# Kernel tuning notes

Hardware: AMD Instinct MI355X
Metric: run time of the kernel (lower is better)

Reference implementation:

```python
import jax, jax.numpy as jnp
import numpy as np

DIM = 1024
HEADS = 16
HDIM = DIM // HEADS  # 64
HID = 4096           # mlp_ratio * dim
SCALE = HDIM ** -0.5
EPS = 1e-5           # torch LayerNorm default


def _ln(z, g, b):
    m = jnp.mean(z, axis=-1, keepdims=True)
    v = jnp.var(z, axis=-1, keepdims=True)
    return (z - m) * jax.lax.rsqrt(v + EPS) * g + b


def _forward(x, g1, beta1, Wq, bq, Wk, bk, Wv, bv, Wo, bo, g2, beta2, W1, b1m, W2, b2m,
             window_size, spatial_h, spatial_w):
    B, L, C = x.shape
    ws = window_size
    nh, nw = spatial_h // ws, spatial_w // ws  # grid divisible by window -> pad = 0

    # norm1 + window partition: [B,L,C] -> [B*nh*nw, ws*ws, C]
    h = _ln(x, g1, beta1).reshape(B, spatial_h, spatial_w, C)
    h = h.reshape(B, nh, ws, nw, ws, C).transpose(0, 1, 3, 2, 4, 5)
    h = h.reshape(B * nh * nw, ws * ws, C)
    Bw, N, _ = h.shape

    # separate q/k/v linears, manual scaled-dot-product attention
    q = (h @ Wq + bq).reshape(Bw, N, HEADS, HDIM).transpose(0, 2, 1, 3)
    k = (h @ Wk + bk).reshape(Bw, N, HEADS, HDIM).transpose(0, 2, 1, 3)
    v = (h @ Wv + bv).reshape(Bw, N, HEADS, HDIM).transpose(0, 2, 1, 3)
    attn = jax.nn.softmax(jnp.einsum('bhqd,bhkd->bhqk', q, k) * SCALE, axis=-1)
    o = jnp.einsum('bhqk,bhkd->bhqd', attn, v).transpose(0, 2, 1, 3).reshape(Bw, N, C)
    o = o @ Wo + bo

    # window unpartition back to [B,L,C]
    o = o.reshape(B, nh, nw, ws, ws, C).transpose(0, 1, 3, 2, 4, 5).reshape(B, L, C)

    x = x + o  # residual (drop_path prob = 0)
    h2 = _ln(x, g2, beta2)
    x = x + (jax.nn.gelu(h2 @ W1 + b1m, approximate=False) @ W2 + b2m)
    return x


def setup_inputs() -> dict:
    key = jax.random.key(0)
    ks = jax.random.split(key, 8)
    s = 0.02
    return {
        'x': jax.random.normal(ks[0], (8, 4096, DIM), jnp.float32),
        'g1': jnp.ones((DIM,), jnp.float32),
        'beta1': jnp.zeros((DIM,), jnp.float32),
        'Wq': jax.random.normal(ks[1], (DIM, DIM), jnp.float32) * s,
        'bq': jnp.zeros((DIM,), jnp.float32),
        'Wk': jax.random.normal(ks[2], (DIM, DIM), jnp.float32) * s,
        'bk': jnp.zeros((DIM,), jnp.float32),
        'Wv': jax.random.normal(ks[3], (DIM, DIM), jnp.float32) * s,
        'bv': jnp.zeros((DIM,), jnp.float32),
        'Wo': jax.random.normal(ks[4], (DIM, DIM), jnp.float32) * s,
        'bo': jnp.zeros((DIM,), jnp.float32),
        'g2': jnp.ones((DIM,), jnp.float32),
        'beta2': jnp.zeros((DIM,), jnp.float32),
        'W1': jax.random.normal(ks[5], (DIM, HID), jnp.float32) * s,
        'b1m': jnp.zeros((HID,), jnp.float32),
        'W2': jax.random.normal(ks[6], (HID, DIM), jnp.float32) * s,
        'b2m': jnp.zeros((DIM,), jnp.float32),
        'window_size': 16,
        'spatial_h': 64,
        'spatial_w': 64,
    }


def reference(x, g1, beta1, Wq, bq, Wk, bk, Wv, bv, Wo, bo, g2, beta2, W1, b1m, W2, b2m,
              window_size, spatial_h, spatial_w):
    return _forward(x, g1, beta1, Wq, bq, Wk, bk, Wv, bv, Wo, bo, g2, beta2,
                    W1, b1m, W2, b2m, window_size, spatial_h, spatial_w)
```

## Files before the change

kernel.cpp:

```cpp
#include <hip/hip_runtime.h>
#include <math.h>
#include <stdint.h>

typedef __bf16 bf16;
typedef __bf16 bf16x8 __attribute__((ext_vector_type(8)));
typedef __bf16 bf16x4 __attribute__((ext_vector_type(4)));
typedef float  f32x4  __attribute__((ext_vector_type(4)));

#define MFMA(a,b,c) __builtin_amdgcn_mfma_f32_16x16x32_bf16(a,b,c,0,0,0)

__device__ __forceinline__ float gelu_exact(float z){
    return 0.5f * z * (1.0f + erff(z * 0.70710678118654752f));
}

__device__ __forceinline__ void gload16(const void* g, void* l){
    __builtin_amdgcn_global_load_lds(
        (const __attribute__((address_space(1))) uint32_t*)(uintptr_t)g,
        (__attribute__((address_space(3))) uint32_t*)(uintptr_t)l,
        16, 0, 0);
}

__global__ void wprep(const float* __restrict__ W, bf16* __restrict__ WT, int K, int N)
{
    __shared__ float tile[32][33];
    int tx = threadIdx.x, ty = threadIdx.y;
    int n0 = blockIdx.x * 32, k0 = blockIdx.y * 32;
    for (int j = 0; j < 4; j++)
        tile[ty + j*8][tx] = W[(size_t)(k0 + ty + j*8) * N + n0 + tx];
    __syncthreads();
    for (int j = 0; j < 4; j++)
        WT[(size_t)(n0 + ty + j*8) * K + k0 + tx] = (bf16)tile[tx][ty + j*8];
}

__global__ void bcat(const float* __restrict__ a, const float* __restrict__ b,
                     const float* __restrict__ c, float* __restrict__ o)
{
    int t = blockIdx.x * 256 + threadIdx.x;
    o[t] = t < 1024 ? a[t] : (t < 2048 ? b[t - 1024] : c[t - 2048]);
}

template<int PERM>
__global__ __launch_bounds__(256) void ln_kernel(const float* __restrict__ x,
    const float* __restrict__ g, const float* __restrict__ beta,
    bf16* __restrict__ out)
{
    int rw = blockIdx.x;
    int src = rw;
    if (PERM){
        int w = rw >> 8, p = rw & 255;
        int b = w >> 4, inh = (w >> 2) & 3, inw = w & 3, pi = p >> 4, pj = p & 15;
        src = b * 4096 + (inh*16 + pi) * 64 + inw*16 + pj;
    }
    const float* xr = x + (size_t)src * 1024;
    int t = threadIdx.x;
    float4 xv = ((const float4*)xr)[t];
    float s  = xv.x + xv.y + xv.z + xv.w;
    float sq = xv.x*xv.x + xv.y*xv.y + xv.z*xv.z + xv.w*xv.w;
    for (int m = 1; m < 64; m <<= 1){ s += __shfl_xor(s, m); sq += __shfl_xor(sq, m); }
    __shared__ float red[8];
    int wid = t >> 6, lane = t & 63;
    if (lane == 0){ red[wid] = s; red[4 + wid] = sq; }
    __syncthreads();
    float S  = red[0] + red[1] + red[2] + red[3];
    float SQ = red[4] + red[5] + red[6] + red[7];
    float mean = S * (1.f/1024.f);
    float var  = SQ * (1.f/1024.f) - mean*mean;
    float rstd = rsqrtf(var + 1e-5f);
    float4 gv = ((const float4*)g)[t];
    float4 bv = ((const float4*)beta)[t];
    bf16x4 o;
    o[0] = (bf16)((xv.x - mean) * rstd * gv.x + bv.x);
    o[1] = (bf16)((xv.y - mean) * rstd * gv.y + bv.y);
    o[2] = (bf16)((xv.z - mean) * rstd * gv.z + bv.z);
    o[3] = (bf16)((xv.w - mean) * rstd * gv.w + bv.w);
    *(bf16x4*)(out + (size_t)rw * 1024 + t*4) = o;
}

template<int EPI>
__global__ __launch_bounds__(512, 2) void gemm256(
    const bf16* __restrict__ Ag, const bf16* __restrict__ BT,
    const float* __restrict__ bias, const float* __restrict__ res,
    void* __restrict__ outp, int N, int K)
{
    extern __shared__ char lds[];
    const int KT = K >> 6;
    const int gx = N >> 8;
    int nwg = gridDim.x;
    int id  = blockIdx.x;
    int cpx = nwg >> 3;
    int wg  = (id & 7) * cpx + (id >> 3);
    int bx = wg % gx, by = wg / gx;
    int m0 = by << 8, n0 = bx << 8;

    int t = threadIdx.x;
    int lane = t & 63, wid = t >> 6;
    int wm = wid >> 2, wn = wid & 3;
    int qoff = lane & 15, quad = lane >> 4;

    auto stage = [&](int H){
        int kt = H >> 2, h = H & 3;
        int isA = h >> 1, hh = h & 1;
        char* lb = lds + ((kt & 1) << 16) + (isA << 15) + (hh << 14);
        const bf16* g0 = (isA ? Ag + (size_t)(m0 + (hh << 7)) * K
                              : BT + (size_t)(n0 + (hh << 7)) * K) + (kt << 6);
        #pragma unroll
        for (int ld = 0; ld < 2; ld++){
            int ch  = ld*512 + t;
            int row = ch >> 3;
            int cc  = (ch & 7) ^ (row & 7);
            gload16(g0 + (size_t)row * K + cc*8, lb + (ld*512 + wid*64)*16);
        }
    };

    f32x4 acc[8][4] = {};

    int npro = 4*KT < 7 ? 4*KT : 7;
    for (int H = 0; H < npro; H++) stage(H);
    asm volatile("s_waitcnt vmcnt(6)" ::: "memory");
    __builtin_amdgcn_s_barrier();
    __builtin_amdgcn_sched_barrier(0);

    const int HMAX = 4*KT;
    const char* lA0 = lds + 32768 + (wm << 14) + qoff*128;
    const char* lB0 = lds + ((wn >> 1) << 14) + ((wn & 1) << 13) + qoff*128;
    int p0 = (quad ^ (qoff & 7)) << 4;
    int p1 = p0 ^ 64;

    for (int kt = 0; kt < KT; kt++){
        int bufo = (kt & 1) << 16;
        const char* lA = lA0 + bufo;
        const char* lB = lB0 + bufo;
        bf16x8 a0[8], a1[8], b0[4], b1[4];

        #pragma unroll
        for (int nt = 0; nt < 4; nt++){
            b0[nt] = *(const bf16x8*)(lB + nt*2048 + p0);
            b1[nt] = *(const bf16x8*)(lB + nt*2048 + p1);
        }
        #pragma unroll
        for (int mt = 0; mt < 8; mt++)
            a0[mt] = *(const bf16x8*)(lA + mt*2048 + p0);
        if (4*kt + 7 < HMAX) stage(4*kt + 7);
        __builtin_amdgcn_sched_barrier(0);
        __builtin_amdgcn_s_barrier();
        __builtin_amdgcn_sched_barrier(0);
        __builtin_amdgcn_s_setprio(1);
        #pragma unroll
        for (int mt = 0; mt < 8; mt++){
            acc[mt][0] = MFMA(a0[mt], b0[0], acc[mt][0]);
            acc[mt][1] = MFMA(a0[mt], b0[1], acc[mt][1]);
        }
        __builtin_amdgcn_s_setprio(0);
        __builtin_amdgcn_sched_barrier(0);
        asm volatile("s_waitcnt lgkmcnt(0)" ::: "memory");
        __builtin_amdgcn_s_barrier();
        __builtin_amdgcn_sched_barrier(0);

        #pragma unroll
        for (int mt = 0; mt < 8; mt++)
            a1[mt] = *(const bf16x8*)(lA + mt*2048 + p1);
        if (4*kt + 8 < HMAX) stage(4*kt + 8);
        __builtin_amdgcn_sched_barrier(0);
        __builtin_amdgcn_s_barrier();
        __builtin_amdgcn_sched_barrier(0);
        __builtin_amdgcn_s_setprio(1);
        #pragma unroll
        for (int mt = 0; mt < 8; mt++){
            acc[mt][2] = MFMA(a0[mt], b0[2], acc[mt][2]);
            acc[mt][3] = MFMA(a0[mt], b0[3], acc[mt][3]);
        }
        __builtin_amdgcn_s_setprio(0);
        __builtin_amdgcn_sched_barrier(0);
        __builtin_amdgcn_s_barrier();
        __builtin_amdgcn_sched_barrier(0);

        if (4*kt + 9 < HMAX) stage(4*kt + 9);
        __builtin_amdgcn_sched_barrier(0);
        __builtin_amdgcn_s_barrier();
        __builtin_amdgcn_sched_barrier(0);
        __builtin_amdgcn_s_setprio(1);
        #pragma unroll
        for (int mt = 0; mt < 8; mt++){
            acc[mt][0] = MFMA(a1[mt], b1[0], acc[mt][0]);
            acc[mt][1] = MFMA(a1[mt], b1[1], acc[mt][1]);
        }
        __builtin_amdgcn_s_setprio(0);
        __builtin_amdgcn_sched_barrier(0);
        __builtin_amdgcn_s_barrier();
        __builtin_amdgcn_sched_barrier(0);

        if (4*kt + 10 < HMAX) stage(4*kt + 10);
        __builtin_amdgcn_sched_barrier(0);
        __builtin_amdgcn_s_barrier();
        __builtin_amdgcn_sched_barrier(0);
        __builtin_amdgcn_s_setprio(1);
        #pragma unroll
        for (int mt = 0; mt < 8; mt++){
            acc[mt][2] = MFMA(a1[mt], b1[2], acc[mt][2]);
            acc[mt][3] = MFMA(a1[mt], b1[3], acc[mt][3]);
        }
        __builtin_amdgcn_s_setprio(0);
        __builtin_amdgcn_sched_barrier(0);
        if (kt + 2 == KT)      asm volatile("s_waitcnt vmcnt(0)" ::: "memory");
        else if (kt + 1 < KT)  asm volatile("s_waitcnt vmcnt(6)" ::: "memory");
        __builtin_amdgcn_s_barrier();
        __builtin_amdgcn_sched_barrier(0);
    }

    #pragma unroll
    for (int mt = 0; mt < 8; mt++){
        #pragma unroll
        for (int reg = 0; reg < 4; reg++){
            int grow = m0 + wm*128 + mt*16 + quad*4 + reg;
            size_t orow = (size_t)grow;
            if (EPI == 2){
                int w = grow >> 8, p = grow & 255;
                int b = w >> 4, inh = (w >> 2) & 3, inw = w & 3, pi = p >> 4, pj = p & 15;
                orow = (size_t)b * 4096 + (inh*16 + pi) * 64 + inw*16 + pj;
            }
            #pragma unroll
            for (int nt = 0; nt < 4; nt++){
                int gcol = n0 + wn*64 + nt*16 + qoff;
                float vv = acc[mt][nt][reg] + bias[gcol];
                if (EPI == 1) vv = gelu_exact(vv);
                if (EPI >= 2) vv += res[orow * (size_t)N + gcol];
                if (EPI <= 1) ((bf16*)outp)[orow * (size_t)N + gcol] = (bf16)vv;
                else          ((float*)outp)[orow * (size_t)N + gcol] = vv;
            }
        }
    }
}

__global__ __launch_bounds__(256) void attn_kernel(
    const bf16* __restrict__ qkv, bf16* __restrict__ ao)
{
    __shared__ bf16 VT[64 * 264];
    __shared__ bf16 Pw[4][16 * 136];
    int wh = blockIdx.x;
    int win = wh >> 4, head = wh & 15;
    size_t base = (size_t)win * 256;
    int cb = head * 64;
    int t = threadIdx.x, lane = t & 63, wv = t >> 6;
    int qoff = lane & 15, quad = lane >> 4;

    const bf16* vb = qkv + base * 3072 + 2048 + cb;
    for (int i = 0; i < 8; i++){
        int c = t + i*256;
        int row = c >> 3, d0 = (c & 7) * 8;
        bf16x8 vvec = *(const bf16x8*)&vb[(size_t)row * 3072 + d0];
        for (int j = 0; j < 8; j++) VT[(d0 + j) * 264 + row] = vvec[j];
    }
    __syncthreads();

    const bf16* qb = qkv + base * 3072 + cb;
    const bf16* kb = qkv + base * 3072 + 1024 + cb;

    for (int qblk = 0; qblk < 4; qblk++){
        int m0 = wv * 64 + qblk * 16;
        bf16x8 aq0 = *(const bf16x8*)&qb[(size_t)(m0 + qoff) * 3072 + quad*8];
        bf16x8 aq1 = *(const bf16x8*)&qb[(size_t)(m0 + qoff) * 3072 + 32 + quad*8];
        f32x4 S[16];
        __builtin_amdgcn_s_setprio(1);
        for (int nt = 0; nt < 16; nt++){
            bf16x8 b0 = *(const bf16x8*)&kb[(size_t)(nt*16 + qoff) * 3072 + quad*8];
            bf16x8 b1 = *(const bf16x8*)&kb[(size_t)(nt*16 + qoff) * 3072 + 32 + quad*8];
            f32x4 a = {0.f, 0.f, 0.f, 0.f};
            a = MFMA(aq0, b0, a);
            a = MFMA(aq1, b1, a);
            S[nt] = a;
        }
        __builtin_amdgcn_s_setprio(0);
        float inv[4];
        for (int r = 0; r < 4; r++){
            float mx = -1e30f;
            for (int nt = 0; nt < 16; nt++) mx = fmaxf(mx, S[nt][r]);
            for (int m = 1; m < 16; m <<= 1) mx = fmaxf(mx, __shfl_xor(mx, m));
            float sum = 0.f;
            for (int nt = 0; nt < 16; nt++){
                float p = __expf((S[nt][r] - mx) * 0.125f);
                S[nt][r] = p; sum += p;
            }
            for (int m = 1; m < 16; m <<= 1) sum += __shfl_xor(sum, m);
            inv[r] = 1.f / sum;
        }
        f32x4 O[4] = {};
        for (int h = 0; h < 2; h++){
            for (int nt = 0; nt < 8; nt++)
                for (int r = 0; r < 4; r++)
                    Pw[wv][(quad*4 + r)*136 + nt*16 + qoff] = (bf16)S[h*8 + nt][r];
            __builtin_amdgcn_s_setprio(1);
            for (int ks = 0; ks < 4; ks++){
                bf16x8 ap = *(bf16x8*)&Pw[wv][qoff*136 + ks*32 + quad*8];
                for (int vt = 0; vt < 4; vt++){
                    bf16x8 bvv = *(bf16x8*)&VT[(vt*16 + qoff)*264 + (h*4 + ks)*32 + quad*8];
                    O[vt] = MFMA(ap, bvv, O[vt]);
                }
            }
            __builtin_amdgcn_s_setprio(0);
        }
        for (int vt = 0; vt < 4; vt++)
            for (int r = 0; r < 4; r++){
                size_t row = base + m0 + quad*4 + r;
                ao[row * 1024 + cb + vt*16 + qoff] = (bf16)(O[vt][r] * inv[r]);
            }
    }
}

extern "C" void kernel_launch(void* const* d_in, const int* in_sizes, int n_in,
                              void* d_out, int out_size, void* d_ws, size_t ws_size,
                              hipStream_t stream)
{
    const float* x     = (const float*)d_in[0];
    const float* g1    = (const float*)d_in[1];
    const float* beta1 = (const float*)d_in[2];
    const float* Wq    = (const float*)d_in[3];
    const float* bq    = (const float*)d_in[4];
    const float* Wk    = (const float*)d_in[5];
    const float* bk    = (const float*)d_in[6];
    const float* Wv    = (const float*)d_in[7];
    const float* bv    = (const float*)d_in[8];
    const float* Wo    = (const float*)d_in[9];
    const float* bo    = (const float*)d_in[10];
    const float* g2    = (const float*)d_in[11];
    const float* beta2 = (const float*)d_in[12];
    const float* W1    = (const float*)d_in[13];
    const float* b1m   = (const float*)d_in[14];
    const float* W2    = (const float*)d_in[15];
    const float* b2m   = (const float*)d_in[16];

    char* ws = (char*)d_ws;
    const size_t MB = 1024ull * 1024ull;
    bf16* WqkvT = (bf16*)(ws + 0*MB);
    bf16* WoT   = (bf16*)(ws + 6*MB);
    bf16* W1T   = (bf16*)(ws + 8*MB);
    bf16* W2T   = (bf16*)(ws + 16*MB);
    bf16* hw    = (bf16*)(ws + 24*MB);
    bf16* qkv   = (bf16*)(ws + 88*MB);
    bf16* ao    = (bf16*)(ws + 24*MB);
    bf16* m1    = (bf16*)(ws + 24*MB);
    float* x2   = (float*)(ws + 280*MB);
    float* bqkv = (float*)(ws + 280*MB);
    bf16* h2    = (bf16*)(ws + 408*MB);

    static bool s_attr = false;
    if (!s_attr){
        s_attr = true;
        hipFuncSetAttribute(reinterpret_cast<const void*>(gemm256<0>),
                            hipFuncAttributeMaxDynamicSharedMemorySize, 131072);
        hipFuncSetAttribute(reinterpret_cast<const void*>(gemm256<1>),
                            hipFuncAttributeMaxDynamicSharedMemorySize, 131072);
        hipFuncSetAttribute(reinterpret_cast<const void*>(gemm256<2>),
                            hipFuncAttributeMaxDynamicSharedMemorySize, 131072);
        hipFuncSetAttribute(reinterpret_cast<const void*>(gemm256<3>),
                            hipFuncAttributeMaxDynamicSharedMemorySize, 131072);
    }

    dim3 tb(32, 8);

    wprep<<<dim3(32, 32),  tb, 0, stream>>>(Wq, WqkvT,              1024, 1024);
    wprep<<<dim3(32, 32),  tb, 0, stream>>>(Wk, WqkvT + 1024*1024,  1024, 1024);
    wprep<<<dim3(32, 32),  tb, 0, stream>>>(Wv, WqkvT + 2048*1024,  1024, 1024);
    wprep<<<dim3(32, 32),  tb, 0, stream>>>(Wo, WoT, 1024, 1024);
    wprep<<<dim3(128, 32), tb, 0, stream>>>(W1, W1T, 1024, 4096);
    wprep<<<dim3(32, 128), tb, 0, stream>>>(W2, W2T, 4096, 1024);
    bcat<<<12, 256, 0, stream>>>(bq, bk, bv, bqkv);

    ln_kernel<1><<<32768, 256, 0, stream>>>(x, g1, beta1, hw);

    gemm256<0><<<12*128, 512, 131072, stream>>>(hw, WqkvT, bqkv, nullptr, qkv, 3072, 1024);

    attn_kernel<<<2048, 256, 0, stream>>>(qkv, ao);

    gemm256<2><<<4*128, 512, 131072, stream>>>(ao, WoT, bo, x, x2, 1024, 1024);

    ln_kernel<0><<<32768, 256, 0, stream>>>(x2, g2, beta2, h2);

    gemm256<1><<<16*128, 512, 131072, stream>>>(h2, W1T, b1m, nullptr, m1, 4096, 1024);
    gemm256<3><<<4*128, 512, 131072, stream>>>(m1, W2T, b2m, x2, (float*)d_out, 1024, 4096);
}
```

Before: 1.515 ms.

## Restructure GEMM main loop to prefetch next-tile LDS fragments and use polynomial erf

The GEMM K-loop is reorganized so each iteration stages the tile two steps ahead and prefetches the next tile's A and B LDS fragments while the current tile's MFMAs run. It also cuts some barriers and waits per iteration. This should hide LDS read latency behind matrix work. Separately, the exact erff in the GELU epilogue is replaced by an Abramowitz-Stegun polynomial approximation with __expf, which lowers epilogue cost but adds approximation error of about 1e-7 absolute.

After: 1.452 ms. 4.2% less time.

```diff
diff --git a/kernel.cpp b/kernel.cpp
--- a/kernel.cpp
+++ b/kernel.cpp
@@ -9,8 +9,16 @@
 
 #define MFMA(a,b,c) __builtin_amdgcn_mfma_f32_16x16x32_bf16(a,b,c,0,0,0)
 
+__device__ __forceinline__ float erf_fast(float x){
+    float ax = fabsf(x);
+    float t = 1.0f / (1.0f + 0.3275911f * ax);
+    float p = t*(0.254829592f + t*(-0.284496736f + t*(1.421413741f +
+              t*(-1.453152027f + t*1.061405429f))));
+    float r = 1.0f - p * __expf(-ax*ax);
+    return copysignf(r, x);
+}
 __device__ __forceinline__ float gelu_exact(float z){
-    return 0.5f * z * (1.0f + erff(z * 0.70710678118654752f));
+    return 0.5f * z * (1.0f + erf_fast(z * 0.70710678118654752f));
 }
 
 __device__ __forceinline__ void gload16(const void* g, void* l){
@@ -97,8 +105,7 @@
     int wm = wid >> 2, wn = wid & 3;
     int qoff = lane & 15, quad = lane >> 4;
 
-    auto stage = [&](int H){
-        int kt = H >> 2, h = H & 3;
+    auto stage = [&](int kt, int h){
         int isA = h >> 1, hh = h & 1;
         char* lb = lds + ((kt & 1) << 16) + (isA << 15) + (hh << 14);
         const bf16* g0 = (isA ? Ag + (size_t)(m0 + (hh << 7)) * K
@@ -113,36 +120,40 @@
     };
 
     f32x4 acc[8][4] = {};
-
-    int npro = 4*KT < 7 ? 4*KT : 7;
-    for (int H = 0; H < npro; H++) stage(H);
-    asm volatile("s_waitcnt vmcnt(6)" ::: "memory");
-    __builtin_amdgcn_s_barrier();
-    __builtin_amdgcn_sched_barrier(0);
-
-    const int HMAX = 4*KT;
+    bf16x8 a0[8], a1[8], b0[4], b1[4];
+
     const char* lA0 = lds + 32768 + (wm << 14) + qoff*128;
     const char* lB0 = lds + ((wn >> 1) << 14) + ((wn & 1) << 13) + qoff*128;
     int p0 = (quad ^ (qoff & 7)) << 4;
     int p1 = p0 ^ 64;
 
-    for (int kt = 0; kt < KT; kt++){
-        int bufo = (kt & 1) << 16;
-        const char* lA = lA0 + bufo;
-        const char* lB = lB0 + bufo;
-        bf16x8 a0[8], a1[8], b0[4], b1[4];
-
-        #pragma unroll
-        for (int nt = 0; nt < 4; nt++){
-            b0[nt] = *(const bf16x8*)(lB + nt*2048 + p0);
-            b1[nt] = *(const bf16x8*)(lB + nt*2048 + p1);
-        }
+    for (int kt = 0; kt < 2; ++kt)
+        for (int h = 0; h < 4; ++h) stage(kt, h);
+    asm volatile("s_waitcnt vmcnt(8)" ::: "memory");
+    __builtin_amdgcn_s_barrier();
+    #pragma unroll
+    for (int mt = 0; mt < 8; mt++) a0[mt] = *(const bf16x8*)(lA0 + mt*2048 + p0);
+    #pragma unroll
+    for (int nt = 0; nt < 4; nt++){
+        b0[nt] = *(const bf16x8*)(lB0 + nt*2048 + p0);
+        b1[nt] = *(const bf16x8*)(lB0 + nt*2048 + p1);
+    }
+    asm volatile("s_waitcnt lgkmcnt(0)" ::: "memory");
+    __builtin_amdgcn_s_barrier();
+
+    for (int j = 0; j < KT; ++j){
+        int cur = (j & 1) << 16;
+        int nxt = cur ^ 0x10000;
+        const char* lA  = lA0 + cur;
+        const char* lAn = lA0 + nxt;
+        const char* lBn = lB0 + nxt;
+        bool sg = (j + 2 < KT);
+        bool rd = (j + 1 < KT);
+
+        if (sg) stage(j+2, 0);
         #pragma unroll
         for (int mt = 0; mt < 8; mt++)
-            a0[mt] = *(const bf16x8*)(lA + mt*2048 + p0);
-        if (4*kt + 7 < HMAX) stage(4*kt + 7);
-        __builtin_amdgcn_sched_barrier(0);
-        __builtin_amdgcn_s_barrier();
+            a1[mt] = *(const bf16x8*)(lA + mt*2048 + p1);
         __builtin_amdgcn_sched_barrier(0);
         __builtin_amdgcn_s_setprio(1);
         #pragma unroll
@@ -152,16 +163,9 @@
         }
         __builtin_amdgcn_s_setprio(0);
         __builtin_amdgcn_sched_barrier(0);
-        asm volatile("s_waitcnt lgkmcnt(0)" ::: "memory");
         __builtin_amdgcn_s_barrier();
-        __builtin_amdgcn_sched_barrier(0);
-
-        #pragma unroll
-        for (int mt = 0; mt < 8; mt++)
-            a1[mt] = *(const bf16x8*)(lA + mt*2048 + p1);
-        if (4*kt + 8 < HMAX) stage(4*kt + 8);
-        __builtin_amdgcn_sched_barrier(0);
-        __builtin_amdgcn_s_barrier();
+
+        if (sg) stage(j+2, 1);
         __builtin_amdgcn_sched_barrier(0);
         __builtin_amdgcn_s_setprio(1);
         #pragma unroll
@@ -171,12 +175,16 @@
         }
         __builtin_amdgcn_s_setprio(0);
         __builtin_amdgcn_sched_barrier(0);
+        if (sg) asm volatile("s_waitcnt lgkmcnt(0) vmcnt(4)" ::: "memory");
+        else    asm volatile("s_waitcnt lgkmcnt(0) vmcnt(0)" ::: "memory");
         __builtin_amdgcn_s_barrier();
-        __builtin_amdgcn_sched_barrier(0);
-
-        if (4*kt + 9 < HMAX) stage(4*kt + 9);
-        __builtin_amdgcn_sched_barrier(0);
-        __builtin_amdgcn_s_barrier();
+
+        if (sg) stage(j+2, 2);
+        if (rd){
+            #pragma unroll
+            for (int mt = 0; mt < 8; mt++)
+                a0[mt] = *(const bf16x8*)(lAn + mt*2048 + p0);
+        }
         __builtin_amdgcn_sched_barrier(0);
         __builtin_amdgcn_s_setprio(1);
         #pragma unroll
@@ -187,11 +195,8 @@
         __builtin_amdgcn_s_setprio(0);
         __builtin_amdgcn_sched_barrier(0);
         __builtin_amdgcn_s_barrier();
-        __builtin_amdgcn_sched_barrier(0);
-
-        if (4*kt + 10 < HMAX) stage(4*kt + 10);
-        __builtin_amdgcn_sched_barrier(0);
-        __builtin_amdgcn_s_barrier();
+
+        if (sg) stage(j+2, 3);
         __builtin_amdgcn_sched_barrier(0);
         __builtin_amdgcn_s_setprio(1);
         #pragma unroll
@@ -201,10 +206,15 @@
         }
         __builtin_amdgcn_s_setprio(0);
         __builtin_amdgcn_sched_barrier(0);
-        if (kt + 2 == KT)      asm volatile("s_waitcnt vmcnt(0)" ::: "memory");
-        else if (kt + 1 < KT)  asm volatile("s_waitcnt vmcnt(6)" ::: "memory");
+        if (rd){
+            #pragma unroll
+            for (int nt = 0; nt < 4; nt++){
+                b0[nt] = *(const bf16x8*)(lBn + nt*2048 + p0);
+                b1[nt] = *(const bf16x8*)(lBn + nt*2048 + p1);
+            }
+            asm volatile("s_waitcnt lgkmcnt(0)" ::: "memory");
+        }
         __builtin_amdgcn_s_barrier();
-        __builtin_amdgcn_sched_barrier(0);
     }
 
     #pragma unroll
```
